# Kernel optimization log

Measured on AMD Instinct MI355X. Metric: run time of the kernel, lower is better.

## Reference

```python
import jax, jax.numpy as jnp
import numpy as np

D = 768      # hidden_size
L = 4        # num_hidden_layers
H = 12       # num_attention_heads
I = 3072     # intermediate_size
B, S = 2, 2048
EPS = 1e-5


def setup_inputs() -> dict:
    key = jax.random.key(0)
    ks = jax.random.split(key, 8)
    sc = 0.02
    return {
        "x": jax.random.normal(ks[0], (B, S, D), dtype=jnp.float32),
        # weights stored as [in, out] so y = x @ W + b (same math as torch Linear)
        "qkv_w": jax.random.normal(ks[1], (L, D, 3 * D), dtype=jnp.float32) * sc,
        "qkv_b": jnp.zeros((L, 3 * D), dtype=jnp.float32),
        "out_w": jax.random.normal(ks[2], (L, D, D), dtype=jnp.float32) * sc,
        "out_b": jnp.zeros((L, D), dtype=jnp.float32),
        "ln1_w": jnp.ones((L, D), dtype=jnp.float32),
        "ln1_b": jnp.zeros((L, D), dtype=jnp.float32),
        "fc1_w": jax.random.normal(ks[3], (L, D, I), dtype=jnp.float32) * sc,
        "fc1_b": jnp.zeros((L, I), dtype=jnp.float32),
        "fc2_w": jax.random.normal(ks[4], (L, I, D), dtype=jnp.float32) * sc,
        "fc2_b": jnp.zeros((L, D), dtype=jnp.float32),
        "ln2_w": jnp.ones((L, D), dtype=jnp.float32),
        "ln2_b": jnp.zeros((L, D), dtype=jnp.float32),
    }


def _layer_norm(x, w, b):
    mu = jnp.mean(x, axis=-1, keepdims=True)
    var = jnp.mean(jnp.square(x - mu), axis=-1, keepdims=True)
    return (x - mu) * jax.lax.rsqrt(var + EPS) * w + b


def _encoder(x, qkv_w, qkv_b, out_w, out_b, ln1_w, ln1_b,
             fc1_w, fc1_b, fc2_w, fc2_b, ln2_w, ln2_b):
    hd = D // H
    scale = 1.0 / jnp.sqrt(jnp.float32(hd))

    def block(x, p):
        (qw, qb, ow, ob, l1w, l1b, f1w, f1b, f2w, f2b, l2w, l2b) = p
        # --- attention sub-block (pre-norm residual) ---
        h = _layer_norm(x, l1w, l1b)
        qkv = h @ qw + qb                      # [B,S,3D]
        qkv = qkv.reshape(B, S, H, 3 * hd).transpose(0, 2, 1, 3)  # [B,H,S,3hd]
        q, k, v = jnp.split(qkv, 3, axis=-1)
        logits = jnp.einsum('bhqd,bhkd->bhqk', q, k) * scale       # [B,H,S,S]
        attn = jax.nn.softmax(logits, axis=-1)
        vals = jnp.einsum('bhqk,bhkd->bhqd', attn, v)              # [B,H,S,hd]
        vals = vals.transpose(0, 2, 1, 3).reshape(B, S, D)
        x = x + vals @ ow + ob
        # --- MLP sub-block (pre-norm residual) ---
        h = _layer_norm(x, l2w, l2b)
        h = jax.nn.gelu(h @ f1w + f1b, approximate=False)
        x = x + h @ f2w + f2b
        return x, None

    params = (qkv_w, qkv_b, out_w, out_b, ln1_w, ln1_b,
              fc1_w, fc1_b, fc2_w, fc2_b, ln2_w, ln2_b)
    x, _ = jax.lax.scan(block, x, params)
    return x


def reference(x, qkv_w, qkv_b, out_w, out_b, ln1_w, ln1_b,
              fc1_w, fc1_b, fc2_w, fc2_b, ln2_w, ln2_b):
    return _encoder(x, qkv_w, qkv_b, out_w, out_b, ln1_w, ln1_b,
                    fc1_w, fc1_b, fc2_w, fc2_b, ln2_w, ln2_b)
```

## Files before the change

kernel.cpp:

```cpp
#include <hip/hip_runtime.h>
#include <stdint.h>
#include <math.h>

#define D_MODEL 768
#define NTOK    4096
#define SEQ     2048
#define NHEAD   12
#define HDIM    64
#define D_FF    3072
#define QKV_N   2304

typedef unsigned short ushort_t;
typedef short  short8 __attribute__((ext_vector_type(8)));
typedef float  f32x4  __attribute__((ext_vector_type(4)));
typedef float  f32x16 __attribute__((ext_vector_type(16)));

__device__ __forceinline__ float b2f(ushort_t u) {
  union { unsigned int u; float f; } v; v.u = ((unsigned int)u) << 16; return v.f;
}
__device__ __forceinline__ ushort_t f2b(float f) {
  union { float f; unsigned int u; } v; v.f = f;
  unsigned int u = v.u;
  return (ushort_t)((u + 0x7fffu + ((u >> 16) & 1u)) >> 16);
}
__device__ __forceinline__ unsigned cvtpk_bf16(float lo, float hi) {
  unsigned r;
  asm("v_cvt_pk_bf16_f32 %0, %1, %2" : "=v"(r) : "v"(lo), "v"(hi));
  return r;
}

__global__ __launch_bounds__(256) void transpose_layer(
    const float* __restrict__ qkv_w, const float* __restrict__ out_w,
    const float* __restrict__ fc1_w, const float* __restrict__ fc2_w,
    ushort_t* __restrict__ qkvT, ushort_t* __restrict__ outT,
    ushort_t* __restrict__ f1T, ushort_t* __restrict__ f2T) {
  __shared__ ushort_t tile[32][33];
  int bid = blockIdx.x;
  const float* src; ushort_t* dst; int K, N, tn, tk;
  if (bid < 1728)      { src = qkv_w; dst = qkvT; K = 768;  N = 2304; tn = bid % 72;  tk = bid / 72; }
  else if (bid < 2304) { int b = bid - 1728; src = out_w; dst = outT; K = 768;  N = 768;  tn = b % 24; tk = b / 24; }
  else if (bid < 4608) { int b = bid - 2304; src = fc1_w; dst = f1T;  K = 768;  N = 3072; tn = b % 96; tk = b / 96; }
  else                 { int b = bid - 4608; src = fc2_w; dst = f2T;  K = 3072; N = 768;  tn = b % 24; tk = b / 24; }
  int n0 = tn * 32, k0 = tk * 32;
  int tx = threadIdx.x, ty = threadIdx.y;
  #pragma unroll
  for (int i = 0; i < 32; i += 8)
    tile[ty + i][tx] = f2b(src[(size_t)(k0 + ty + i) * N + n0 + tx]);
  __syncthreads();
  #pragma unroll
  for (int i = 0; i < 32; i += 8)
    dst[(size_t)(n0 + ty + i) * K + k0 + tx] = tile[tx][ty + i];
}

__global__ __launch_bounds__(256) void ln_kernel(const float* __restrict__ x,
                                                 const float* __restrict__ w,
                                                 const float* __restrict__ b,
                                                 ushort_t* __restrict__ out) {
  __shared__ float red[4];
  int tok = blockIdx.x, t = threadIdx.x;
  const float* xr = x + (size_t)tok * D_MODEL;
  float v0 = xr[t], v1 = xr[t + 256], v2 = xr[t + 512];
  float s = v0 + v1 + v2;
  #pragma unroll
  for (int o = 1; o < 64; o <<= 1) s += __shfl_xor(s, o, 64);
  if ((t & 63) == 0) red[t >> 6] = s;
  __syncthreads();
  float mean = (red[0] + red[1] + red[2] + red[3]) * (1.0f / 768.0f);
  __syncthreads();
  float d0 = v0 - mean, d1 = v1 - mean, d2 = v2 - mean;
  float q = d0 * d0 + d1 * d1 + d2 * d2;
  #pragma unroll
  for (int o = 1; o < 64; o <<= 1) q += __shfl_xor(q, o, 64);
  if ((t & 63) == 0) red[t >> 6] = q;
  __syncthreads();
  float var = (red[0] + red[1] + red[2] + red[3]) * (1.0f / 768.0f);
  float rs = rsqrtf(var + 1e-5f);
  ushort_t* orow = out + (size_t)tok * D_MODEL;
  orow[t]       = f2b(d0 * rs * w[t]       + b[t]);
  orow[t + 256] = f2b(d1 * rs * w[t + 256] + b[t + 256]);
  orow[t + 512] = f2b(d2 * rs * w[t + 512] + b[t + 512]);
}

template <int EPI, int TN>
__global__ __launch_bounds__(256) void gemm_kernel(
    const ushort_t* __restrict__ A, const ushort_t* __restrict__ BT,
    const float* __restrict__ bias, const float* __restrict__ resid,
    float* __restrict__ Cf, ushort_t* __restrict__ Cb, int M, int N, int K) {
  constexpr int NI = (TN == 128) ? 4 : 2;
  __shared__ ushort_t As[2][128 * 32];
  __shared__ ushort_t Bs[2][TN * 32];
  int t = threadIdx.x;
  int lane = t & 63, wave = t >> 6;
  int gx = gridDim.x;
  int nwg = gx * gridDim.y;
  int bid0 = blockIdx.y * gx + blockIdx.x;
  int qn = nwg >> 3, rm = nwg & 7;
  int xcd = bid0 & 7, pos = bid0 >> 3;
  int wg = (xcd < rm ? xcd * (qn + 1) : rm * (qn + 1) + (xcd - rm) * qn) + pos;
  int m0 = (wg / gx) * 128, n0 = (wg % gx) * TN;
  int wm = (TN == 128) ? (wave & 1) * 64 : wave * 32;
  int wn = (TN == 128) ? (wave >> 1) * 64 : 0;
  int quad = lane >> 4, l16 = lane & 15;
  int kq = quad * 8;
  int lrow = lane >> 2, lcol = (lane & 3) * 8;

  auto stage = [&](int k0, int buf) {
    #pragma unroll
    for (int c = 0; c < 2; ++c) {
      int rowA = wave * 32 + c * 16 + lrow;
      const ushort_t* ga = A + (size_t)(m0 + rowA) * K + k0 + lcol;
      ushort_t* la = &As[buf][(wave * 32 + c * 16) * 32];
      __builtin_amdgcn_global_load_lds((const __attribute__((address_space(1))) void*)ga,
                                       (__attribute__((address_space(3))) void*)la, 16, 0, 0);
      if (TN == 128 || c == 0) {
        int rowB = (TN == 128) ? rowA : (wave * 16 + lrow);
        const ushort_t* gb = BT + (size_t)(n0 + rowB) * K + k0 + lcol;
        ushort_t* lb = (TN == 128) ? &Bs[buf][(wave * 32 + c * 16) * 32]
                                   : &Bs[buf][(wave * 16) * 32];
        __builtin_amdgcn_global_load_lds((const __attribute__((address_space(1))) void*)gb,
                                         (__attribute__((address_space(3))) void*)lb, 16, 0, 0);
      }
    }
  };

  f32x4 acc[NI][4];
  #pragma unroll
  for (int i = 0; i < NI; ++i)
    #pragma unroll
    for (int j = 0; j < 4; ++j) acc[i][j] = (f32x4){0.f, 0.f, 0.f, 0.f};

  stage(0, 0);
  int nk = K / 32;
  for (int ki = 0; ki < nk; ++ki) {
    int cur = ki & 1;
    __syncthreads();
    if (ki + 1 < nk) stage((ki + 1) * 32, cur ^ 1);
    short8 af[NI], bf[4];
    #pragma unroll
    for (int i = 0; i < NI; ++i)
      af[i] = *(const short8*)&As[cur][(wm + i * 16 + l16) * 32 + kq];
    #pragma unroll
    for (int j = 0; j < 4; ++j)
      bf[j] = *(const short8*)&Bs[cur][(wn + j * 16 + l16) * 32 + kq];
    #pragma unroll
    for (int i = 0; i < NI; ++i)
      #pragma unroll
      for (int j = 0; j < 4; ++j)
        acc[i][j] = __builtin_amdgcn_mfma_f32_16x16x32_bf16(af[i], bf[j], acc[i][j], 0, 0, 0);
  }

  #pragma unroll
  for (int i = 0; i < NI; ++i) {
    #pragma unroll
    for (int j = 0; j < 4; ++j) {
      int col = n0 + wn + j * 16 + l16;
      float bv = bias[col];
      #pragma unroll
      for (int r = 0; r < 4; ++r) {
        int row = m0 + wm + i * 16 + quad * 4 + r;
        float v = acc[i][j][r] + bv;
        if (EPI == 1) v = 0.5f * v * (1.0f + erff(v * 0.70710678118654752f));
        if (EPI == 2) v += resid[(size_t)row * N + col];
        if (EPI == 2) Cf[(size_t)row * N + col] = v;
        else          Cb[(size_t)row * N + col] = f2b(v);
      }
    }
  }
}

__global__ __launch_bounds__(256, 3) void attn_kernel(const ushort_t* __restrict__ qkv,
                                                      ushort_t* __restrict__ out) {
  __shared__ __align__(16) ushort_t Ks[2][64 * 72];
  __shared__ __align__(16) ushort_t Vt[2][64 * 72];
  int t = threadIdx.x;
  int lane = t & 63, wave = t >> 6;
  int l31 = lane & 31, h = lane >> 5, h8 = h * 8;
  int kh = wave & 1, qh = wave >> 1;
  int kw = kh * 32;
  int qt = blockIdx.x;
  int bh = blockIdx.y;
  int b = bh / NHEAD, hd = bh % NHEAD;
  size_t base = (size_t)b * SEQ * QKV_N + hd * 192;

  const float kscale = 0.125f * 1.44269504088896f;

  short8 qf[4];
  {
    const ushort_t* qp = qkv + base + (size_t)(qt * 64 + qh * 32 + l31) * QKV_N + h8;
    #pragma unroll
    for (int ks = 0; ks < 4; ++ks) qf[ks] = *(const short8*)(qp + ks * 16);
  }

  int krow = t >> 1, kcol = (t & 1) * 32;
  int kcb = krow >> 6, krl = krow & 63;
  int kp = t & 63, vdb = (t >> 6) * 16;
  int vcb = kp >> 5, kpl = kp & 31;
  short8 kr[4], va[2], vb[2];
  auto kv_load = [&](int sbase) {
    const ushort_t* gk = qkv + base + (size_t)(sbase + krow) * QKV_N + 64 + kcol;
    #pragma unroll
    for (int i = 0; i < 4; ++i) kr[i] = *(const short8*)(gk + i * 8);
    const ushort_t* gv = qkv + base + (size_t)(sbase + 2 * kp) * QKV_N + 128 + vdb;
    va[0] = *(const short8*)gv;           va[1] = *(const short8*)(gv + 8);
    vb[0] = *(const short8*)(gv + QKV_N); vb[1] = *(const short8*)(gv + QKV_N + 8);
  };
  auto kv_write = [&]() {
    #pragma unroll
    for (int i = 0; i < 4; ++i)
      *(short8*)&Ks[kcb][krl * 72 + kcol + i * 8] = kr[i];
    unsigned* vtw = (unsigned*)&Vt[vcb][0];
    #pragma unroll
    for (int half = 0; half < 2; ++half)
      #pragma unroll
      for (int e = 0; e < 8; ++e) {
        unsigned pk = (unsigned)(unsigned short)va[half][e] |
                      ((unsigned)(unsigned short)vb[half][e] << 16);
        vtw[(vdb + half * 8 + e) * 36 + kpl] = pk;
      }
  };

  f32x16 o0, o1;
  #pragma unroll
  for (int i = 0; i < 16; ++i) { o0[i] = 0.f; o1[i] = 0.f; }
  float ls = 0.f;

  kv_load(0);
  for (int it = 0; it < SEQ / 128; ++it) {
    kv_write();
    __syncthreads();
    if (it + 1 < SEQ / 128) kv_load((it + 1) * 128);

    #pragma unroll
    for (int c = 0; c < 2; ++c) {
      f32x16 s;
      #pragma unroll
      for (int i = 0; i < 16; ++i) s[i] = 0.f;
      __builtin_amdgcn_s_setprio(1);
      #pragma unroll
      for (int ks = 0; ks < 4; ++ks) {
        short8 kf = *(const short8*)&Ks[c][(kw + l31) * 72 + ks * 16 + h8];
        s = __builtin_amdgcn_mfma_f32_32x32x16_bf16(kf, qf[ks], s, 0, 0, 0);
      }
      __builtin_amdgcn_s_setprio(0);

      unsigned wpk[4][2];
      #pragma unroll
      for (int g = 0; g < 4; ++g) {
        float p0 = exp2f(s[4 * g + 0] * kscale), p1 = exp2f(s[4 * g + 1] * kscale);
        float p2 = exp2f(s[4 * g + 2] * kscale), p3 = exp2f(s[4 * g + 3] * kscale);
        ls += (p0 + p1) + (p2 + p3);
        wpk[g][0] = cvtpk_bf16(p0, p1);
        wpk[g][1] = cvtpk_bf16(p2, p3);
      }

      #pragma unroll
      for (int k4 = 0; k4 < 2; ++k4) {
        int j2 = k4 * 2;
        unsigned f[4];
        #pragma unroll
        for (int c2 = 0; c2 < 2; ++c2) {
          unsigned a  = wpk[j2][c2];
          unsigned b2 = wpk[j2 + 1][c2];
          unsigned snd = h ? a : b2;
          unsigned rcv = (unsigned)__shfl_xor((int)snd, 32, 64);
          f[c2]     = h ? rcv : a;
          f[2 + c2] = h ? b2 : rcv;
        }
        union { unsigned u[4]; short8 s8; } uc;
        uc.u[0] = f[0]; uc.u[1] = f[1]; uc.u[2] = f[2]; uc.u[3] = f[3];
        short8 ap = uc.s8;
        short8 v0 = *(const short8*)&Vt[c][(l31)      * 72 + kw + k4 * 16 + h8];
        short8 v1 = *(const short8*)&Vt[c][(32 + l31) * 72 + kw + k4 * 16 + h8];
        __builtin_amdgcn_s_setprio(1);
        o0 = __builtin_amdgcn_mfma_f32_32x32x16_bf16(ap, v0, o0, 0, 0, 0);
        o1 = __builtin_amdgcn_mfma_f32_32x32x16_bf16(ap, v1, o1, 0, 0, 0);
        __builtin_amdgcn_s_setprio(0);
      }
    }
    __syncthreads();
  }

  float* slab = (float*)&Ks[0][0];
  if (kh == 1) {
    float* s = slab + (size_t)(qh * 64 + lane) * 33;
    #pragma unroll
    for (int i = 0; i < 16; ++i) { s[i] = o0[i]; s[16 + i] = o1[i]; }
    s[32] = ls;
  }
  __syncthreads();
  if (kh == 0) {
    float* s = slab + (size_t)(qh * 64 + lane) * 33;
    #pragma unroll
    for (int i = 0; i < 16; ++i) { o0[i] += s[i]; o1[i] += s[16 + i]; }
    ls += s[32];
    ls += __shfl_xor(ls, 32, 64);

    size_t ob = (size_t)(b * SEQ + qt * 64 + qh * 32) * D_MODEL + hd * HDIM;
    #pragma unroll
    for (int g = 0; g < 4; ++g) {
      #pragma unroll
      for (int r = 0; r < 4; ++r) {
        int reg = 4 * g + r;
        int qrow = 8 * g + 4 * h + r;
        float inv = 1.0f / __shfl(ls, qrow, 64);
        ushort_t* orow = out + ob + (size_t)qrow * D_MODEL;
        orow[l31]      = f2b(o0[reg] * inv);
        orow[32 + l31] = f2b(o1[reg] * inv);
      }
    }
  }
}

extern "C" void kernel_launch(void* const* d_in, const int* in_sizes, int n_in,
                              void* d_out, int out_size, void* d_ws, size_t ws_size,
                              hipStream_t stream) {
  const float* x_in  = (const float*)d_in[0];
  const float* qkv_w = (const float*)d_in[1];
  const float* qkv_b = (const float*)d_in[2];
  const float* out_w = (const float*)d_in[3];
  const float* out_b = (const float*)d_in[4];
  const float* ln1_w = (const float*)d_in[5];
  const float* ln1_b = (const float*)d_in[6];
  const float* fc1_w = (const float*)d_in[7];
  const float* fc1_b = (const float*)d_in[8];
  const float* fc2_w = (const float*)d_in[9];
  const float* fc2_b = (const float*)d_in[10];
  const float* ln2_w = (const float*)d_in[11];
  const float* ln2_b = (const float*)d_in[12];

  char* ws = (char*)d_ws;
  size_t off = 0;
  auto alloc = [&](size_t bytes) -> void* {
    void* p = ws + off; off += (bytes + 255) & ~(size_t)255; return p;
  };
  float*    buf_x  = (float*)   alloc((size_t)NTOK * D_MODEL * 4);
  float*    buf_x2 = (float*)   alloc((size_t)NTOK * D_MODEL * 4);
  ushort_t* bigb   = (ushort_t*)alloc((size_t)NTOK * D_FF * 2);
  ushort_t* h_b    = (ushort_t*)alloc((size_t)NTOK * D_MODEL * 2);
  ushort_t* at_b   = (ushort_t*)alloc((size_t)NTOK * D_MODEL * 2);
  ushort_t* qkvT   = (ushort_t*)alloc((size_t)QKV_N * D_MODEL * 2);
  ushort_t* outT   = (ushort_t*)alloc((size_t)D_MODEL * D_MODEL * 2);
  ushort_t* f1T    = (ushort_t*)alloc((size_t)D_FF * D_MODEL * 2);
  ushort_t* f2T    = (ushort_t*)alloc((size_t)D_MODEL * D_FF * 2);

  ushort_t* qkv_a = bigb;
  ushort_t* mlp_b = bigb;

  for (int l = 0; l < 4; ++l) {
    const float* resid_in = (l == 0) ? x_in : buf_x;
    transpose_layer<<<6912, dim3(32, 8), 0, stream>>>(
        qkv_w + (size_t)l * D_MODEL * QKV_N, out_w + (size_t)l * D_MODEL * D_MODEL,
        fc1_w + (size_t)l * D_MODEL * D_FF,  fc2_w + (size_t)l * D_FF * D_MODEL,
        qkvT, outT, f1T, f2T);
    ln_kernel<<<NTOK, 256, 0, stream>>>(resid_in, ln1_w + l * D_MODEL, ln1_b + l * D_MODEL, h_b);
    gemm_kernel<0, 128><<<dim3(QKV_N / 128, NTOK / 128), 256, 0, stream>>>(
        h_b, qkvT, qkv_b + l * QKV_N, nullptr, nullptr, qkv_a, NTOK, QKV_N, D_MODEL);
    attn_kernel<<<dim3(SEQ / 64, 2 * NHEAD), 256, 0, stream>>>(qkv_a, at_b);
    gemm_kernel<2, 64><<<dim3(D_MODEL / 64, NTOK / 128), 256, 0, stream>>>(
        at_b, outT, out_b + l * D_MODEL, resid_in, buf_x2, nullptr, NTOK, D_MODEL, D_MODEL);
    ln_kernel<<<NTOK, 256, 0, stream>>>(buf_x2, ln2_w + l * D_MODEL, ln2_b + l * D_MODEL, h_b);
    gemm_kernel<1, 128><<<dim3(D_FF / 128, NTOK / 128), 256, 0, stream>>>(
        h_b, f1T, fc1_b + l * D_FF, nullptr, nullptr, mlp_b, NTOK, D_FF, D_MODEL);
    float* x_next = (l < 3) ? buf_x : (float*)d_out;
    gemm_kernel<2, 64><<<dim3(D_MODEL / 64, NTOK / 128), 256, 0, stream>>>(
        mlp_b, f2T, fc2_b + l * D_MODEL, buf_x2, x_next, nullptr, NTOK, D_MODEL, D_FF);
  }
  (void)in_sizes; (void)n_in; (void)out_size; (void)ws_size;
}
```

Before: 960.3 us.

## Restructure attention to 32-query blocks with direct-global K and folded Q scale

Measured after the change: 1.128 ms. +17.4%, slower.

```diff
diff --git a/kernel.cpp b/kernel.cpp
--- a/kernel.cpp
+++ b/kernel.cpp
@@ -155,10 +155,13 @@
     for (int j = 0; j < 4; ++j) {
       int col = n0 + wn + j * 16 + l16;
       float bv = bias[col];
+      float sc = 1.0f;
+      if (EPI == 0) sc = ((col % 192) < 64) ? 0.18033688011112043f : 1.0f;
       #pragma unroll
       for (int r = 0; r < 4; ++r) {
         int row = m0 + wm + i * 16 + quad * 4 + r;
         float v = acc[i][j][r] + bv;
+        if (EPI == 0) v *= sc;
         if (EPI == 1) v = 0.5f * v * (1.0f + erff(v * 0.70710678118654752f));
         if (EPI == 2) v += resid[(size_t)row * N + col];
         if (EPI == 2) Cf[(size_t)row * N + col] = v;
@@ -168,54 +171,42 @@
   }
 }
 
-__global__ __launch_bounds__(256, 3) void attn_kernel(const ushort_t* __restrict__ qkv,
+#define KP 136
+__global__ __launch_bounds__(256, 4) void attn_kernel(const ushort_t* __restrict__ qkv,
                                                       ushort_t* __restrict__ out) {
-  __shared__ __align__(16) ushort_t Ks[2][64 * 72];
-  __shared__ __align__(16) ushort_t Vt[2][64 * 72];
+  __shared__ __align__(16) ushort_t Vt[64 * KP];
   int t = threadIdx.x;
   int lane = t & 63, wave = t >> 6;
   int l31 = lane & 31, h = lane >> 5, h8 = h * 8;
-  int kh = wave & 1, qh = wave >> 1;
-  int kw = kh * 32;
+  int kw = wave * 32;
   int qt = blockIdx.x;
   int bh = blockIdx.y;
   int b = bh / NHEAD, hd = bh % NHEAD;
   size_t base = (size_t)b * SEQ * QKV_N + hd * 192;
 
-  const float kscale = 0.125f * 1.44269504088896f;
-
   short8 qf[4];
   {
-    const ushort_t* qp = qkv + base + (size_t)(qt * 64 + qh * 32 + l31) * QKV_N + h8;
+    const ushort_t* qp = qkv + base + (size_t)(qt * 32 + l31) * QKV_N + h8;
     #pragma unroll
     for (int ks = 0; ks < 4; ++ks) qf[ks] = *(const short8*)(qp + ks * 16);
   }
 
-  int krow = t >> 1, kcol = (t & 1) * 32;
-  int kcb = krow >> 6, krl = krow & 63;
-  int kp = t & 63, vdb = (t >> 6) * 16;
-  int vcb = kp >> 5, kpl = kp & 31;
-  short8 kr[4], va[2], vb[2];
-  auto kv_load = [&](int sbase) {
-    const ushort_t* gk = qkv + base + (size_t)(sbase + krow) * QKV_N + 64 + kcol;
-    #pragma unroll
-    for (int i = 0; i < 4; ++i) kr[i] = *(const short8*)(gk + i * 8);
+  int kp = lane, vdb = wave * 16;
+  short8 va[2], vb[2];
+  auto v_load = [&](int sbase) {
     const ushort_t* gv = qkv + base + (size_t)(sbase + 2 * kp) * QKV_N + 128 + vdb;
     va[0] = *(const short8*)gv;           va[1] = *(const short8*)(gv + 8);
     vb[0] = *(const short8*)(gv + QKV_N); vb[1] = *(const short8*)(gv + QKV_N + 8);
   };
-  auto kv_write = [&]() {
-    #pragma unroll
-    for (int i = 0; i < 4; ++i)
-      *(short8*)&Ks[kcb][krl * 72 + kcol + i * 8] = kr[i];
-    unsigned* vtw = (unsigned*)&Vt[vcb][0];
+  auto v_write = [&]() {
+    unsigned* vtw = (unsigned*)&Vt[0];
     #pragma unroll
     for (int half = 0; half < 2; ++half)
       #pragma unroll
       for (int e = 0; e < 8; ++e) {
-        unsigned pk = (unsigned)(unsigned short)va[half][e] |
-                      ((unsigned)(unsigned short)vb[half][e] << 16);
-        vtw[(vdb + half * 8 + e) * 36 + kpl] = pk;
+        unsigned pk2 = (unsigned)(unsigned short)va[half][e] |
+                       ((unsigned)(unsigned short)vb[half][e] << 16);
+        vtw[(vdb + half * 8 + e) * (KP / 2) + kp] = pk2;
       }
   };
 
@@ -224,78 +215,97 @@
   for (int i = 0; i < 16; ++i) { o0[i] = 0.f; o1[i] = 0.f; }
   float ls = 0.f;
 
-  kv_load(0);
-  for (int it = 0; it < SEQ / 128; ++it) {
-    kv_write();
+  v_load(0);
+  const int NSS = SEQ / 128;
+  for (int it = 0; it < NSS; ++it) {
+    v_write();
     __syncthreads();
-    if (it + 1 < SEQ / 128) kv_load((it + 1) * 128);
-
-    #pragma unroll
-    for (int c = 0; c < 2; ++c) {
-      f32x16 s;
-      #pragma unroll
-      for (int i = 0; i < 16; ++i) s[i] = 0.f;
+    int sb = it * 128;
+
+    short8 kf[4];
+    {
+      const ushort_t* gk = qkv + base + (size_t)(sb + kw + l31) * QKV_N + 64 + h8;
+      #pragma unroll
+      for (int ks = 0; ks < 4; ++ks) kf[ks] = *(const short8*)(gk + ks * 16);
+    }
+    if (it + 1 < NSS) v_load(sb + 128);
+
+    f32x16 s;
+    #pragma unroll
+    for (int i = 0; i < 16; ++i) s[i] = 0.f;
+    __builtin_amdgcn_s_setprio(1);
+    #pragma unroll
+    for (int ks = 0; ks < 4; ++ks)
+      s = __builtin_amdgcn_mfma_f32_32x32x16_bf16(kf[ks], qf[ks], s, 0, 0, 0);
+    __builtin_amdgcn_s_setprio(0);
+
+    unsigned wpk[4][2];
+    #pragma unroll
+    for (int g = 0; g < 4; ++g) {
+      float p0 = exp2f(s[4 * g + 0]), p1 = exp2f(s[4 * g + 1]);
+      float p2 = exp2f(s[4 * g + 2]), p3 = exp2f(s[4 * g + 3]);
+      ls += (p0 + p1) + (p2 + p3);
+      wpk[g][0] = cvtpk_bf16(p0, p1);
+      wpk[g][1] = cvtpk_bf16(p2, p3);
+    }
+
+    #pragma unroll
+    for (int k4 = 0; k4 < 2; ++k4) {
+      int j2 = k4 * 2;
+      unsigned f0, f1, f2, f3;
+      {
+        unsigned x = wpk[j2][0], y = wpk[j2 + 1][0];
+        asm("v_permlane32_swap_b32 %0, %1" : "+v"(y), "+v"(x));
+        f0 = x; f2 = y;
+      }
+      {
+        unsigned x = wpk[j2][1], y = wpk[j2 + 1][1];
+        asm("v_permlane32_swap_b32 %0, %1" : "+v"(y), "+v"(x));
+        f1 = x; f3 = y;
+      }
+      union { unsigned u[4]; short8 s8; } uc;
+      uc.u[0] = f0; uc.u[1] = f1; uc.u[2] = f2; uc.u[3] = f3;
+      short8 ap = uc.s8;
+      short8 v0 = *(const short8*)&Vt[(size_t)(l31)      * KP + kw + k4 * 16 + h8];
+      short8 v1 = *(const short8*)&Vt[(size_t)(32 + l31) * KP + kw + k4 * 16 + h8];
       __builtin_amdgcn_s_setprio(1);
-      #pragma unroll
-      for (int ks = 0; ks < 4; ++ks) {
-        short8 kf = *(const short8*)&Ks[c][(kw + l31) * 72 + ks * 16 + h8];
-        s = __builtin_amdgcn_mfma_f32_32x32x16_bf16(kf, qf[ks], s, 0, 0, 0);
-      }
+      o0 = __builtin_amdgcn_mfma_f32_32x32x16_bf16(ap, v0, o0, 0, 0, 0);
+      o1 = __builtin_amdgcn_mfma_f32_32x32x16_bf16(ap, v1, o1, 0, 0, 0);
       __builtin_amdgcn_s_setprio(0);
-
-      unsigned wpk[4][2];
-      #pragma unroll
-      for (int g = 0; g < 4; ++g) {
-        float p0 = exp2f(s[4 * g + 0] * kscale), p1 = exp2f(s[4 * g + 1] * kscale);
-        float p2 = exp2f(s[4 * g + 2] * kscale), p3 = exp2f(s[4 * g + 3] * kscale);
-        ls += (p0 + p1) + (p2 + p3);
-        wpk[g][0] = cvtpk_bf16(p0, p1);
-        wpk[g][1] = cvtpk_bf16(p2, p3);
-      }
-
-      #pragma unroll
-      for (int k4 = 0; k4 < 2; ++k4) {
-        int j2 = k4 * 2;
-        unsigned f[4];
-        #pragma unroll
-        for (int c2 = 0; c2 < 2; ++c2) {
-          unsigned a  = wpk[j2][c2];
-          unsigned b2 = wpk[j2 + 1][c2];
-          unsigned snd = h ? a : b2;
-          unsigned rcv = (unsigned)__shfl_xor((int)snd, 32, 64);
-          f[c2]     = h ? rcv : a;
-          f[2 + c2] = h ? b2 : rcv;
-        }
-        union { unsigned u[4]; short8 s8; } uc;
-        uc.u[0] = f[0]; uc.u[1] = f[1]; uc.u[2] = f[2]; uc.u[3] = f[3];
-        short8 ap = uc.s8;
-        short8 v0 = *(const short8*)&Vt[c][(l31)      * 72 + kw + k4 * 16 + h8];
-        short8 v1 = *(const short8*)&Vt[c][(32 + l31) * 72 + kw + k4 * 16 + h8];
-        __builtin_amdgcn_s_setprio(1);
-        o0 = __builtin_amdgcn_mfma_f32_32x32x16_bf16(ap, v0, o0, 0, 0, 0);
-        o1 = __builtin_amdgcn_mfma_f32_32x32x16_bf16(ap, v1, o1, 0, 0, 0);
-        __builtin_amdgcn_s_setprio(0);
-      }
     }
     __syncthreads();
   }
 
-  float* slab = (float*)&Ks[0][0];
-  if (kh == 1) {
-    float* s = slab + (size_t)(qh * 64 + lane) * 33;
+  float* slab = (float*)&Vt[0];
+  if (wave >= 2) {
+    float* s = slab + (size_t)((wave - 2) * 64 + lane) * 33;
     #pragma unroll
     for (int i = 0; i < 16; ++i) { s[i] = o0[i]; s[16 + i] = o1[i]; }
     s[32] = ls;
   }
   __syncthreads();
-  if (kh == 0) {
-    float* s = slab + (size_t)(qh * 64 + lane) * 33;
+  if (wave < 2) {
+    float* s = slab + (size_t)(wave * 64 + lane) * 33;
+    #pragma unroll
+    for (int i = 0; i < 16; ++i) { o0[i] += s[i]; o1[i] += s[16 + i]; }
+    ls += s[32];
+  }
+  __syncthreads();
+  if (wave == 1) {
+    float* s = slab + (size_t)lane * 33;
+    #pragma unroll
+    for (int i = 0; i < 16; ++i) { s[i] = o0[i]; s[16 + i] = o1[i]; }
+    s[32] = ls;
+  }
+  __syncthreads();
+  if (wave == 0) {
+    float* s = slab + (size_t)lane * 33;
     #pragma unroll
     for (int i = 0; i < 16; ++i) { o0[i] += s[i]; o1[i] += s[16 + i]; }
     ls += s[32];
     ls += __shfl_xor(ls, 32, 64);
 
-    size_t ob = (size_t)(b * SEQ + qt * 64 + qh * 32) * D_MODEL + hd * HDIM;
+    size_t ob = (size_t)(b * SEQ + qt * 32) * D_MODEL + hd * HDIM;
     #pragma unroll
     for (int g = 0; g < 4; ++g) {
       #pragma unroll
@@ -355,7 +365,7 @@
     ln_kernel<<<NTOK, 256, 0, stream>>>(resid_in, ln1_w + l * D_MODEL, ln1_b + l * D_MODEL, h_b);
     gemm_kernel<0, 128><<<dim3(QKV_N / 128, NTOK / 128), 256, 0, stream>>>(
         h_b, qkvT, qkv_b + l * QKV_N, nullptr, nullptr, qkv_a, NTOK, QKV_N, D_MODEL);
-    attn_kernel<<<dim3(SEQ / 64, 2 * NHEAD), 256, 0, stream>>>(qkv_a, at_b);
+    attn_kernel<<<dim3(SEQ / 32, 2 * NHEAD), 256, 0, stream>>>(qkv_a, at_b);
     gemm_kernel<2, 64><<<dim3(D_MODEL / 64, NTOK / 128), 256, 0, stream>>>(
         at_b, outT, out_b + l * D_MODEL, resid_in, buf_x2, nullptr, NTOK, D_MODEL, D_MODEL);
     ln_kernel<<<NTOK, 256, 0, stream>>>(buf_x2, ln2_w + l * D_MODEL, ln2_b + l * D_MODEL, h_b);
```
